# Performance work log

Hardware: AMD Instinct MI355X
Metric: run time of the kernel (lower is better)

## Reference

```python
import jax, jax.numpy as jnp
import numpy as np
from jax import lax

# Straight-through sign: forward sign(x), backward passes grad where |x|<=1 (hardtanh STE)
@jax.custom_vjp
def sign_ste(x):
    return jnp.sign(x)

def _sign_fwd(x):
    return jnp.sign(x), x

def _sign_bwd(x, g):
    return (g * (jnp.abs(x) <= 1.0).astype(g.dtype),)

sign_ste.defvjp(_sign_fwd, _sign_bwd)

STRIDE = 1
PADDING = 1

def setup_inputs() -> dict:
    key = jax.random.key(0)
    k1, k2, k3 = jax.random.split(key, 3)
    B, Cin, H, W = 32, 256, 56, 56
    Cout, K = 256, 3
    inp = jax.random.normal(k1, (B, Cin, H, W), dtype=jnp.float32)
    # kaiming-uniform-ish init like torch Conv2d default
    fan_in = Cin * K * K
    bound = 1.0 / np.sqrt(fan_in)
    weight1 = jax.random.uniform(k2, (Cout, Cin, K, K), minval=-bound, maxval=bound, dtype=jnp.float32)
    weight2 = jax.random.uniform(k3, (Cout, Cin, K, K), minval=-bound, maxval=bound, dtype=jnp.float32)
    return {"input": inp, "weight1": weight1, "weight2": weight2}

def reference(input, weight1, weight2):
    # ternarized weight: (sign(w1)+sign(w2))/2 in {-1,-0.5,0,0.5,1}
    w_ter = (sign_ste(weight1) + sign_ste(weight2)) * 0.5
    x_bin = sign_ste(input)
    out = lax.conv_general_dilated(
        x_bin, w_ter,
        window_strides=(STRIDE, STRIDE),
        padding=[(PADDING, PADDING), (PADDING, PADDING)],
        dimension_numbers=("NCHW", "OIHW", "NCHW"),
    )
    # per-output-channel scaling: mean|w1| + mean|w2| over (in, kh, kw)
    alpha = jnp.mean(jnp.abs(weight1), axis=(1, 2, 3)) + jnp.mean(jnp.abs(weight2), axis=(1, 2, 3))
    return out * alpha[None, :, None, None]
```

## Files before the change

kernel.cpp:

```cpp
#include <hip/hip_runtime.h>
#include <hip/hip_bf16.h>

#define B_    32
#define C_    256
#define H_    56
#define W_    56
#define HP    58
#define WPAD  58
#define HW    3136
#define CHW   802816
#define M_TOT 100352

typedef int intx4 __attribute__((ext_vector_type(4)));

#define XPAD_BYTES (B_ * HP * WPAD * C_)
#define WPK_BYTES  (C_ * 9 * C_)

__device__ __forceinline__ int sgn8(float f) {
  return ((f > 0.f) ? 1 : ((f < 0.f) ? -1 : 0)) & 0xff;
}

#define ROWPC 272
__global__ __launch_bounds__(256) void pack_kernel(const float* __restrict__ in,
                                                   const float* __restrict__ w1,
                                                   const float* __restrict__ w2,
                                                   char* __restrict__ xp,
                                                   char* __restrict__ wq,
                                                   float* __restrict__ alphah) {
  __shared__ char smem[18448];
  const int tid = threadIdx.x;

  if (blockIdx.x < B_ * HP) {
    char* row = smem;
    const int yp = blockIdx.x % HP;
    const int b  = blockIdx.x / HP;

    float4* rz = (float4*)row;
    const float4 z4 = make_float4(0.f, 0.f, 0.f, 0.f);
#pragma unroll
    for (int i = 0; i < 4; ++i) {
      const int idx = i * 256 + tid;
      if (idx < (58 * ROWPC) / 16) rz[idx] = z4;
    }
    __syncthreads();

    const int y = yp - 1;
    const int xq = tid % 14;
    const int cs = tid / 14;
    if (y >= 0 && y < H_ && cs < 18) {
      const float* base = in + ((size_t)b * C_ * H_ + (size_t)y) * W_ + xq * 4;
#pragma unroll
      for (int k = 0; k < 4; ++k) {
        const int cq = cs + 18 * k;
        if (cq < 64) {
          float4 f[4];
#pragma unroll
          for (int j = 0; j < 4; ++j)
            f[j] = *(const float4*)(base + (size_t)(cq * 4 + j) * (H_ * W_));
#pragma unroll
          for (int d = 0; d < 4; ++d) {
            const float v0 = (d == 0) ? f[0].x : (d == 1) ? f[0].y : (d == 2) ? f[0].z : f[0].w;
            const float v1 = (d == 0) ? f[1].x : (d == 1) ? f[1].y : (d == 2) ? f[1].z : f[1].w;
            const float v2 = (d == 0) ? f[2].x : (d == 1) ? f[2].y : (d == 2) ? f[2].z : f[2].w;
            const float v3 = (d == 0) ? f[3].x : (d == 1) ? f[3].y : (d == 2) ? f[3].z : f[3].w;
            const unsigned int pk = (unsigned)sgn8(v0) | ((unsigned)sgn8(v1) << 8) |
                                    ((unsigned)sgn8(v2) << 16) | ((unsigned)sgn8(v3) << 24);
            *(unsigned int*)&row[(xq * 4 + d + 1) * ROWPC + cq * 4] = pk;
          }
        }
      }
    }
    __syncthreads();

    const int cc = tid & 15;
    const int xo = tid >> 4;
    char* dst = xp + (size_t)(b * HP + yp) * WPAD * C_;
#pragma unroll
    for (int it = 0; it < 4; ++it) {
      const int xs = it * 16 + xo;
      if (xs < WPAD)
        *(float4*)(dst + xs * C_ + cc * 16) = *(const float4*)&row[xs * ROWPC + cc * 16];
    }
  } else {
    float* l1 = (float*)smem;
    float* l2 = l1 + 2304;
    float* red = (float*)(smem + 18432);
    const int co = blockIdx.x - B_ * HP;
    const float* s1 = w1 + co * 2304;
    const float* s2 = w2 + co * 2304;
#pragma unroll
    for (int i = 0; i < 9; ++i) {
      l1[i * 256 + tid] = s1[i * 256 + tid];
      l2[i * 256 + tid] = s2[i * 256 + tid];
    }
    __syncthreads();
    const int ci = tid;
    float sabs = 0.f;
#pragma unroll
    for (int s = 0; s < 9; ++s) {
      const float a = l1[ci * 9 + s];
      const float b = l2[ci * 9 + s];
      const int sa = (a > 0.f) - (a < 0.f);
      const int sb = (b > 0.f) - (b < 0.f);
      wq[(co * 9 + s) * C_ + ci] = (char)(sa + sb);
      sabs += fabsf(a) + fabsf(b);
    }
#pragma unroll
    for (int off = 32; off > 0; off >>= 1) sabs += __shfl_down(sabs, off, 64);
    if ((tid & 63) == 0) red[tid >> 6] = sabs;
    __syncthreads();
    if (tid == 0)
      alphah[co] = (red[0] + red[1] + red[2] + red[3]) * (0.5f / 2304.0f);
  }
}

#define GLL16(src, dst)                                                        \
  __builtin_amdgcn_global_load_lds(                                            \
      (const __attribute__((address_space(1))) void*)(src),                    \
      (__attribute__((address_space(3))) void*)(dst), 16, 0, 0)

__global__ __launch_bounds__(256, 2) void gemm_kernel(const char* __restrict__ xp,
                                                      const char* __restrict__ wq,
                                                      const float* __restrict__ alphah,
                                                      float* __restrict__ out) {
  __shared__ char sA[2 * 128 * 64];
  __shared__ char sB[2 * 256 * 64];
  const int tid = threadIdx.x;

  const int id = blockIdx.x;
  const int xcd = id & 7;
  const int l = id >> 3;
  const int co0 = (l & 1) * 128;
  const int m0 = ((l >> 1) * 8 + xcd) * 256;

  const int srow = tid >> 2;
  const int scol = (tid & 3) ^ ((tid >> 3) & 3);

  const char* wsrc[2];
#pragma unroll
  for (int i = 0; i < 2; ++i)
    wsrc[i] = wq + (co0 + srow + 64 * i) * 2304 + scol * 16;
  const char* xsrc[4];
#pragma unroll
  for (int i = 0; i < 4; ++i) {
    const int m = m0 + srow + 64 * i;
    const int b = m / HW;
    const int rem = m - b * HW;
    const int y = rem / W_;
    const int x = rem - y * W_;
    xsrc[i] = xp + ((b * HP + y) * WPAD + x) * C_ + scol * 16;
  }

  auto stage = [&](int s) {
    const int tap = s >> 2;
    const int q = s & 3;
    const int woff = tap * 256 + q * 64;
    const int shoff = ((tap / 3) * WPAD + (tap % 3)) * C_ + q * 64;
    char* dA = sA + (s & 1) * 8192 + tid * 16;
    char* dB = sB + (s & 1) * 16384 + tid * 16;
#pragma unroll
    for (int i = 0; i < 2; ++i)
      GLL16(wsrc[i] + woff, dA + i * 4096);
#pragma unroll
    for (int i = 0; i < 4; ++i)
      GLL16(xsrc[i] + shoff, dB + i * 4096);
  };

  const int lane = tid & 63;
  const int wn = tid >> 6;
  const int lrow = lane & 15;
  const int kq = lane >> 4;
  const int coff = (kq ^ ((lrow >> 1) & 3)) * 16;
  const int abase = lrow * 64 + coff;
  const int bbase = (wn * 64 + lrow) * 64 + coff;

  intx4 acc[8][4] = {};

  stage(0);
#pragma unroll 1
  for (int t = 0; t < 36; ++t) {
    __syncthreads();
    if (t < 35) stage(t + 1);
    const char* bA = sA + (t & 1) * 8192;
    const char* bB = sB + (t & 1) * 16384;
    intx4 af[8], bv[4];
#pragma unroll
    for (int ii = 0; ii < 8; ++ii)
      af[ii] = *(const intx4*)(bA + abase + ii * 1024);
#pragma unroll
    for (int j = 0; j < 4; ++j)
      bv[j] = *(const intx4*)(bB + bbase + j * 1024);
    __builtin_amdgcn_s_setprio(1);
#pragma unroll
    for (int ii = 0; ii < 8; ++ii)
#pragma unroll
      for (int j = 0; j < 4; ++j)
        acc[ii][j] = __builtin_amdgcn_mfma_i32_16x16x64_i8(af[ii], bv[j],
                                                           acc[ii][j], 0, 0, 0);
    __builtin_amdgcn_s_setprio(0);
  }

  int ob[4];
#pragma unroll
  for (int j = 0; j < 4; ++j) {
    const int m = m0 + wn * 64 + j * 16 + lrow;
    const int b = m / HW;
    const int rem = m - b * HW;
    const int y = rem / W_;
    const int x = rem - y * W_;
    ob[j] = b * CHW + y * W_ + x;
  }
#pragma unroll
  for (int ii = 0; ii < 8; ++ii) {
#pragma unroll
    for (int r = 0; r < 4; ++r) {
      const int co = co0 + ii * 16 + kq * 4 + r;
      const float sc = alphah[co];
#pragma unroll
      for (int j = 0; j < 4; ++j)
        out[ob[j] + co * HW] = (float)acc[ii][j][r] * sc;
    }
  }
}

extern "C" void kernel_launch(void* const* d_in, const int* in_sizes, int n_in,
                              void* d_out, int out_size, void* d_ws, size_t ws_size,
                              hipStream_t stream) {
  const float* input = (const float*)d_in[0];
  const float* w1 = (const float*)d_in[1];
  const float* w2 = (const float*)d_in[2];
  float* out = (float*)d_out;

  char* ws = (char*)d_ws;
  char* xp = ws;
  char* wq = ws + XPAD_BYTES;
  float* alphah = (float*)(ws + XPAD_BYTES + WPK_BYTES);

  pack_kernel<<<B_ * HP + C_, 256, 0, stream>>>(input, w1, w2, xp, wq, alphah);
  gemm_kernel<<<784, 256, 0, stream>>>(xp, wq, alphah, out);
}
```

Before: 259.6 us.

## Load activations directly to registers and stage only weights in LDS per tap

The GEMM kernel now uses a 128x128 output tile with a 2x2 wave layout. Activation fragments are read straight from global memory into registers for each of the 9 taps (full 256-channel K per tap), and only the weight tile is double-buffered in LDS with an XOR swizzle. This cuts the main-loop iterations and barriers from 36 to 9 and removes the LDS staging of activations. In exchange, activations reuse less across waves and the grid doubles, so more global/L2 traffic and higher register pressure (64 B fragments per thread) may hurt occupancy.

```diff
diff --git a/kernel.cpp b/kernel.cpp
--- a/kernel.cpp
+++ b/kernel.cpp
@@ -123,81 +123,80 @@
                                                       const char* __restrict__ wq,
                                                       const float* __restrict__ alphah,
                                                       float* __restrict__ out) {
-  __shared__ char sA[2 * 128 * 64];
-  __shared__ char sB[2 * 256 * 64];
+  __shared__ char sA[2 * 128 * 256];
   const int tid = threadIdx.x;
 
   const int id = blockIdx.x;
   const int xcd = id & 7;
   const int l = id >> 3;
   const int co0 = (l & 1) * 128;
-  const int m0 = ((l >> 1) * 8 + xcd) * 256;
-
-  const int srow = tid >> 2;
-  const int scol = (tid & 3) ^ ((tid >> 3) & 3);
-
-  const char* wsrc[2];
-#pragma unroll
-  for (int i = 0; i < 2; ++i)
-    wsrc[i] = wq + (co0 + srow + 64 * i) * 2304 + scol * 16;
-  const char* xsrc[4];
-#pragma unroll
-  for (int i = 0; i < 4; ++i) {
-    const int m = m0 + srow + 64 * i;
+  const int m0 = ((l >> 1) * 8 + xcd) * 128;
+
+  const int srow16 = tid >> 4;
+  const int schunk = (tid & 15) ^ srow16;
+  const char* awsrc = wq + (co0 + srow16) * 2304 + schunk * 16;
+
+  auto stageA = [&](int t, int buf) {
+    const int off = t * 256;
+    char* d = sA + buf * 32768 + tid * 16;
+#pragma unroll
+    for (int i = 0; i < 8; ++i)
+      GLL16(awsrc + off + i * 36864, d + i * 4096);
+  };
+
+  const int lane = tid & 63;
+  const int wave = tid >> 6;
+  const int wm = wave >> 1;
+  const int wn = wave & 1;
+  const int lrow = lane & 15;
+  const int kq = lane >> 4;
+
+  const char* xrow[4];
+#pragma unroll
+  for (int j = 0; j < 4; ++j) {
+    const int m = m0 + wn * 64 + j * 16 + lrow;
     const int b = m / HW;
     const int rem = m - b * HW;
     const int y = rem / W_;
     const int x = rem - y * W_;
-    xsrc[i] = xp + ((b * HP + y) * WPAD + x) * C_ + scol * 16;
-  }
-
-  auto stage = [&](int s) {
-    const int tap = s >> 2;
-    const int q = s & 3;
-    const int woff = tap * 256 + q * 64;
-    const int shoff = ((tap / 3) * WPAD + (tap % 3)) * C_ + q * 64;
-    char* dA = sA + (s & 1) * 8192 + tid * 16;
-    char* dB = sB + (s & 1) * 16384 + tid * 16;
-#pragma unroll
-    for (int i = 0; i < 2; ++i)
-      GLL16(wsrc[i] + woff, dA + i * 4096);
-#pragma unroll
-    for (int i = 0; i < 4; ++i)
-      GLL16(xsrc[i] + shoff, dB + i * 4096);
-  };
-
-  const int lane = tid & 63;
-  const int wn = tid >> 6;
-  const int lrow = lane & 15;
-  const int kq = lane >> 4;
-  const int coff = (kq ^ ((lrow >> 1) & 3)) * 16;
-  const int abase = lrow * 64 + coff;
-  const int bbase = (wn * 64 + lrow) * 64 + coff;
-
-  intx4 acc[8][4] = {};
-
-  stage(0);
+    xrow[j] = xp + ((b * HP + y) * WPAD + x) * C_ + kq * 16;
+  }
+
+  const int abase = (wm * 64 + lrow) * 256;
+
+  intx4 acc[4][4] = {};
+
+  stageA(0, 0);
 #pragma unroll 1
-  for (int t = 0; t < 36; ++t) {
-    __syncthreads();
-    if (t < 35) stage(t + 1);
-    const char* bA = sA + (t & 1) * 8192;
-    const char* bB = sB + (t & 1) * 16384;
-    intx4 af[8], bv[4];
-#pragma unroll
-    for (int ii = 0; ii < 8; ++ii)
-      af[ii] = *(const intx4*)(bA + abase + ii * 1024);
-#pragma unroll
-    for (int j = 0; j < 4; ++j)
-      bv[j] = *(const intx4*)(bB + bbase + j * 1024);
-    __builtin_amdgcn_s_setprio(1);
-#pragma unroll
-    for (int ii = 0; ii < 8; ++ii)
+  for (int t = 0; t < 9; ++t) {
+    __syncthreads();
+    const int shoff = ((t / 3) * WPAD + (t % 3)) * C_;
+
+    intx4 bv[4][4];
+#pragma unroll
+    for (int q = 0; q < 4; ++q)
 #pragma unroll
       for (int j = 0; j < 4; ++j)
-        acc[ii][j] = __builtin_amdgcn_mfma_i32_16x16x64_i8(af[ii], bv[j],
-                                                           acc[ii][j], 0, 0, 0);
-    __builtin_amdgcn_s_setprio(0);
+        bv[q][j] = *(const intx4*)(xrow[j] + shoff + q * 64);
+
+    if (t < 8) stageA(t + 1, (t + 1) & 1);
+
+    const char* bA = sA + (t & 1) * 32768 + abase;
+#pragma unroll
+    for (int q = 0; q < 4; ++q) {
+      intx4 af[4];
+#pragma unroll
+      for (int ii = 0; ii < 4; ++ii)
+        af[ii] = *(const intx4*)(bA + ii * 4096 + (((q * 4 + kq) ^ lrow) * 16));
+      __builtin_amdgcn_s_setprio(1);
+#pragma unroll
+      for (int ii = 0; ii < 4; ++ii)
+#pragma unroll
+        for (int j = 0; j < 4; ++j)
+          acc[ii][j] = __builtin_amdgcn_mfma_i32_16x16x64_i8(af[ii], bv[q][j],
+                                                             acc[ii][j], 0, 0, 0);
+      __builtin_amdgcn_s_setprio(0);
+    }
   }
 
   int ob[4];
@@ -211,10 +210,10 @@
     ob[j] = b * CHW + y * W_ + x;
   }
 #pragma unroll
-  for (int ii = 0; ii < 8; ++ii) {
+  for (int ii = 0; ii < 4; ++ii) {
 #pragma unroll
     for (int r = 0; r < 4; ++r) {
-      const int co = co0 + ii * 16 + kq * 4 + r;
+      const int co = co0 + wm * 64 + ii * 16 + kq * 4 + r;
       const float sc = alphah[co];
 #pragma unroll
       for (int j = 0; j < 4; ++j)
@@ -237,5 +236,5 @@
   float* alphah = (float*)(ws + XPAD_BYTES + WPK_BYTES);
 
   pack_kernel<<<B_ * HP + C_, 256, 0, stream>>>(input, w1, w2, xp, wq, alphah);
-  gemm_kernel<<<784, 256, 0, stream>>>(xp, wq, alphah, out);
-}
+  gemm_kernel<<<1568, 256, 0, stream>>>(xp, wq, alphah, out);
+}
```

Result: slower. 325.2 us (+25.3%).

## Shrink GEMM tile to 128x128 with 2x2 waves and triple-buffered async loads

Applied to the files above, without the earlier changes.

The block tile along M drops from 256 to 128, so twice as many blocks launch (1568), and the four waves are arranged 2x2 over the 128x128 output tile instead of 1x4. Shared-memory staging goes from two buffers to three. Loads are issued two steps ahead, with an explicit vmcnt wait before a bare barrier instead of __syncthreads, and the s_setprio hints are removed. The aim is better latency hiding and occupancy through smaller accumulators and deeper prefetch, at the cost of less data reuse per block and more redundant weight loads.

```diff
diff --git a/kernel.cpp b/kernel.cpp
--- a/kernel.cpp
+++ b/kernel.cpp
@@ -123,26 +123,24 @@
                                                       const char* __restrict__ wq,
                                                       const float* __restrict__ alphah,
                                                       float* __restrict__ out) {
-  __shared__ char sA[2 * 128 * 64];
-  __shared__ char sB[2 * 256 * 64];
+  __shared__ char sA[3 * 128 * 64];
+  __shared__ char sB[3 * 128 * 64];
   const int tid = threadIdx.x;
 
   const int id = blockIdx.x;
   const int xcd = id & 7;
   const int l = id >> 3;
   const int co0 = (l & 1) * 128;
-  const int m0 = ((l >> 1) * 8 + xcd) * 256;
+  const int m0 = ((l >> 1) * 8 + xcd) * 128;
 
   const int srow = tid >> 2;
   const int scol = (tid & 3) ^ ((tid >> 3) & 3);
 
   const char* wsrc[2];
-#pragma unroll
-  for (int i = 0; i < 2; ++i)
+  const char* xsrc[2];
+#pragma unroll
+  for (int i = 0; i < 2; ++i) {
     wsrc[i] = wq + (co0 + srow + 64 * i) * 2304 + scol * 16;
-  const char* xsrc[4];
-#pragma unroll
-  for (int i = 0; i < 4; ++i) {
     const int m = m0 + srow + 64 * i;
     const int b = m / HW;
     const int rem = m - b * HW;
@@ -151,54 +149,68 @@
     xsrc[i] = xp + ((b * HP + y) * WPAD + x) * C_ + scol * 16;
   }
 
-  auto stage = [&](int s) {
+  auto stage = [&](int s, char* dA, char* dB) {
     const int tap = s >> 2;
     const int q = s & 3;
     const int woff = tap * 256 + q * 64;
     const int shoff = ((tap / 3) * WPAD + (tap % 3)) * C_ + q * 64;
-    char* dA = sA + (s & 1) * 8192 + tid * 16;
-    char* dB = sB + (s & 1) * 16384 + tid * 16;
-#pragma unroll
-    for (int i = 0; i < 2; ++i)
-      GLL16(wsrc[i] + woff, dA + i * 4096);
-#pragma unroll
-    for (int i = 0; i < 4; ++i)
-      GLL16(xsrc[i] + shoff, dB + i * 4096);
+    GLL16(wsrc[0] + woff, dA);
+    GLL16(wsrc[1] + woff, dA + 4096);
+    GLL16(xsrc[0] + shoff, dB);
+    GLL16(xsrc[1] + shoff, dB + 4096);
   };
 
   const int lane = tid & 63;
-  const int wn = tid >> 6;
+  const int wave = tid >> 6;
+  const int wm = wave >> 1;
+  const int wn = wave & 1;
   const int lrow = lane & 15;
   const int kq = lane >> 4;
   const int coff = (kq ^ ((lrow >> 1) & 3)) * 16;
-  const int abase = lrow * 64 + coff;
+  const int abase = (wm * 64 + lrow) * 64 + coff;
   const int bbase = (wn * 64 + lrow) * 64 + coff;
 
-  intx4 acc[8][4] = {};
-
-  stage(0);
-#pragma unroll 1
-  for (int t = 0; t < 36; ++t) {
-    __syncthreads();
-    if (t < 35) stage(t + 1);
-    const char* bA = sA + (t & 1) * 8192;
-    const char* bB = sB + (t & 1) * 16384;
-    intx4 af[8], bv[4];
-#pragma unroll
-    for (int ii = 0; ii < 8; ++ii)
-      af[ii] = *(const intx4*)(bA + abase + ii * 1024);
-#pragma unroll
-    for (int j = 0; j < 4; ++j)
-      bv[j] = *(const intx4*)(bB + bbase + j * 1024);
-    __builtin_amdgcn_s_setprio(1);
-#pragma unroll
-    for (int ii = 0; ii < 8; ++ii)
-#pragma unroll
-      for (int j = 0; j < 4; ++j)
-        acc[ii][j] = __builtin_amdgcn_mfma_i32_16x16x64_i8(af[ii], bv[j],
-                                                           acc[ii][j], 0, 0, 0);
-    __builtin_amdgcn_s_setprio(0);
-  }
+  intx4 acc[4][4] = {};
+
+#define STEP(T, CBUF, SBUF, VM, DOSTAGE)                                       \
+  do {                                                                         \
+    asm volatile("s_waitcnt vmcnt(" #VM ")" ::: "memory");                     \
+    __builtin_amdgcn_s_barrier();                                              \
+    asm volatile("" ::: "memory");                                             \
+    if (DOSTAGE)                                                               \
+      stage((T) + 2, sA + (SBUF) * 8192 + tid * 16,                            \
+            sB + (SBUF) * 8192 + tid * 16);                                    \
+    const char* bA = sA + (CBUF) * 8192;                                       \
+    const char* bB = sB + (CBUF) * 8192;                                       \
+    intx4 af[4], bv[4];                                                        \
+    _Pragma("unroll")                                                          \
+    for (int ii = 0; ii < 4; ++ii)                                             \
+      af[ii] = *(const intx4*)(bA + abase + ii * 1024);                        \
+    _Pragma("unroll")                                                          \
+    for (int j = 0; j < 4; ++j)                                                \
+      bv[j] = *(const intx4*)(bB + bbase + j * 1024);                          \
+    _Pragma("unroll")                                                          \
+    for (int ii = 0; ii < 4; ++ii)                                             \
+      _Pragma("unroll")                                                        \
+      for (int j = 0; j < 4; ++j)                                              \
+        acc[ii][j] = __builtin_amdgcn_mfma_i32_16x16x64_i8(af[ii], bv[j],      \
+                                                           acc[ii][j], 0, 0, 0); \
+  } while (0)
+
+  stage(0, sA + tid * 16, sB + tid * 16);
+  asm volatile("" ::: "memory");
+  stage(1, sA + 8192 + tid * 16, sB + 8192 + tid * 16);
+
+  for (int it = 0; it < 11; ++it) {
+    const int t = it * 3;
+    STEP(t, 0, 2, 4, 1);
+    STEP(t + 1, 1, 0, 4, 1);
+    STEP(t + 2, 2, 1, 4, 1);
+  }
+  STEP(33, 0, 2, 4, 1);
+  STEP(34, 1, 0, 4, 0);
+  STEP(35, 2, 1, 0, 0);
+#undef STEP
 
   int ob[4];
 #pragma unroll
@@ -211,10 +223,10 @@
     ob[j] = b * CHW + y * W_ + x;
   }
 #pragma unroll
-  for (int ii = 0; ii < 8; ++ii) {
+  for (int ii = 0; ii < 4; ++ii) {
 #pragma unroll
     for (int r = 0; r < 4; ++r) {
-      const int co = co0 + ii * 16 + kq * 4 + r;
+      const int co = co0 + wm * 64 + ii * 16 + kq * 4 + r;
       const float sc = alphah[co];
 #pragma unroll
       for (int j = 0; j < 4; ++j)
@@ -237,5 +249,5 @@
   float* alphah = (float*)(ws + XPAD_BYTES + WPK_BYTES);
 
   pack_kernel<<<B_ * HP + C_, 256, 0, stream>>>(input, w1, w2, xp, wq, alphah);
-  gemm_kernel<<<784, 256, 0, stream>>>(xp, wq, alphah, out);
-}
+  gemm_kernel<<<M_TOT / 128 * (C_ / 128), 256, 0, stream>>>(xp, wq, alphah, out);
+}
```

After: 261.6 us. No clear change (+0.7%).
